# Performance work log

Hardware: AMD Instinct MI355X
Metric: run time of the kernel (lower is better)

The kernel has to match this reference:

```python
import jax, jax.numpy as jnp
import numpy as np

N_NODES = 100000

def _gcn_conv(x, edge_index, W, b):
    # PyG GCNConv with normalize=False, add_self_loops=False:
    # out[dst] = sum_{(src,dst) in E} (x @ W)[src] + b
    xw = x @ W                                   # [N, out]
    src, dst = edge_index[0], edge_index[1]
    agg = jax.ops.segment_sum(xw[src], dst, num_segments=x.shape[0])  # [N, out]
    return agg + b

def setup_inputs() -> dict:
    key = jax.random.key(0)
    k1, k2, k3, k4 = jax.random.split(key, 4)
    F_in, F_hid, F_out = 128, 64, 40
    E = 1_600_000
    x = jax.random.normal(k1, (N_NODES, F_in), dtype=jnp.float32)
    edge_index = jax.random.randint(k2, (2, E), 0, N_NODES, dtype=jnp.int64)
    W1 = jax.random.normal(k3, (F_in, F_hid), dtype=jnp.float32) * (1.0 / np.sqrt(F_in))
    b1 = jnp.zeros((F_hid,), dtype=jnp.float32)
    W2 = jax.random.normal(k4, (F_hid, F_out), dtype=jnp.float32) * (1.0 / np.sqrt(F_hid))
    b2 = jnp.zeros((F_out,), dtype=jnp.float32)
    return {"x": x, "edge_index": edge_index, "W1": W1, "b1": b1, "W2": W2, "b2": b2}

def reference(x, edge_index, W1, b1, W2, b2):
    h = _gcn_conv(x, edge_index, W1, b1)
    h = jax.nn.relu(h)
    h = _gcn_conv(h, edge_index, W2, b2)
    return jax.nn.log_softmax(h, axis=1)
```

## Files before the change

kernel.cpp:

```cpp
#include <hip/hip_runtime.h>
#include <cstdint>
#include <cstddef>

#define F_IN  128
#define F_HID 64
#define F_OUT 40

#define BSH   9
#define NBMAX 256
#define CHUNK 4096

#define BLD_T   512
#define BLD_CAP 10240

typedef __attribute__((ext_vector_type(8))) short short8;
typedef __attribute__((ext_vector_type(4))) float f32x4;

__device__ __forceinline__ unsigned short f2bf(float f) {
  unsigned u = __float_as_uint(f);
  u += 0x7fffu + ((u >> 16) & 1u);
  return (unsigned short)(u >> 16);
}
__device__ __forceinline__ float bf2f(unsigned short b) {
  return __uint_as_float((unsigned)b << 16);
}
__device__ __forceinline__ float bflo(unsigned u) { return __uint_as_float(u << 16); }
__device__ __forceinline__ float bfhi(unsigned u) { return __uint_as_float(u & 0xffff0000u); }
__device__ __forceinline__ unsigned packbf(float lo, float hi) {
  return (unsigned)f2bf(lo) | ((unsigned)f2bf(hi) << 16);
}

__global__ __launch_bounds__(256) void front_k(const float* __restrict__ x,
                                               const float* __restrict__ W1,
                                               const float* __restrict__ W2,
                                               unsigned short* __restrict__ w2s,
                                               unsigned short* __restrict__ xw, int N,
                                               const int* __restrict__ ei,
                                               int* __restrict__ counts,
                                               int E, int NBLK, int NBUCK) {
  __shared__ int lh[NBMAX];
  __shared__ unsigned short w1l[8192];
  int t = threadIdx.x;

  if ((int)blockIdx.x < NBLK) {
    int blk = blockIdx.x;
    lh[t] = 0;
    __syncthreads();
    int e0 = blk * CHUNK;
    int n = min(CHUNK, E - e0);
    for (int i = t; i < n; i += 256)
      atomicAdd(&lh[((unsigned)ei[E + e0 + i]) >> BSH], 1);
    __syncthreads();
    if (t < NBUCK) counts[t * NBLK + blk] = lh[t];
    if (blk == 0) {
      for (int i = t; i < 3072; i += 256) {
        int f = i >> 9, r = i & 511;
        int lane = r >> 3, j = r & 7;
        int ct = f >> 1, ks = f & 1;
        int n2 = ct * 16 + (lane & 15);
        int k = ks * 32 + (lane >> 4) * 8 + j;
        w2s[i] = (n2 < F_OUT) ? f2bf(W2[k * F_OUT + n2]) : (unsigned short)0;
      }
    }
    return;
  }

  {
    int k = t >> 1, n0 = (t & 1) * 32;
    const float4* wp = (const float4*)(W1 + k * F_HID + n0);
    float4 v[8];
#pragma unroll
    for (int u = 0; u < 8; ++u) v[u] = wp[u];
#pragma unroll
    for (int u = 0; u < 32; ++u) {
      int n = n0 + u;
      float f = ((const float*)v)[u];
      int idx = ((n >> 4) * 4 + (k >> 5)) * 512 +
                (((k >> 3) & 3) * 16 + (n & 15)) * 8 + (k & 7);
      w1l[idx] = f2bf(f);
    }
  }
  __syncthreads();

  int gblk = blockIdx.x - NBLK;
  int lane = t & 63;
  int wid  = gblk * 4 + (t >> 6);
  int row0 = wid * 16;
  if (row0 >= N) return;
  int m = lane & 15, q = lane >> 4;

  if (row0 + 16 <= N) {
    short8 b[16];
#pragma unroll
    for (int f = 0; f < 16; ++f)
      b[f] = *(const short8*)(w1l + f * 512 + lane * 8);

    short8 a[4];
#pragma unroll
    for (int ks = 0; ks < 4; ++ks) {
      const float* xp = x + (size_t)(row0 + m) * F_IN + ks * 32 + q * 8;
      float4 v0 = *(const float4*)xp;
      float4 v1 = *(const float4*)(xp + 4);
      short8 tt;
      tt[0] = (short)f2bf(v0.x); tt[1] = (short)f2bf(v0.y);
      tt[2] = (short)f2bf(v0.z); tt[3] = (short)f2bf(v0.w);
      tt[4] = (short)f2bf(v1.x); tt[5] = (short)f2bf(v1.y);
      tt[6] = (short)f2bf(v1.z); tt[7] = (short)f2bf(v1.w);
      a[ks] = tt;
    }

    f32x4 z = {0.f, 0.f, 0.f, 0.f};
    f32x4 acc[4] = {z, z, z, z};
#pragma unroll
    for (int ct = 0; ct < 4; ++ct)
#pragma unroll
      for (int ks = 0; ks < 4; ++ks)
        acc[ct] = __builtin_amdgcn_mfma_f32_16x16x32_bf16(a[ks], b[ct * 4 + ks],
                                                          acc[ct], 0, 0, 0);
#pragma unroll
    for (int ct = 0; ct < 4; ++ct)
#pragma unroll
      for (int r = 0; r < 4; ++r) {
        int row = row0 + q * 4 + r;
        xw[(size_t)row * F_HID + ct * 16 + m] = f2bf(acc[ct][r]);
      }
  } else {
    for (int r = 0; r < 16 && row0 + r < N; ++r) {
      const float* xr = x + (size_t)(row0 + r) * F_IN;
      float s = 0.f;
      for (int k = 0; k < F_IN; ++k) s = fmaf(xr[k], W1[k * F_HID + lane], s);
      xw[(size_t)(row0 + r) * F_HID + lane] = f2bf(s);
    }
  }
}

__global__ __launch_bounds__(256) void scanA_k(const int* __restrict__ a,
                                               int* __restrict__ psum, int M) {
  int t = threadIdx.x;
  int base = blockIdx.x * 2048 + t * 8;
  int s = 0;
#pragma unroll
  for (int j = 0; j < 8; ++j) if (base + j < M) s += a[base + j];
#pragma unroll
  for (int off = 32; off; off >>= 1) s += __shfl_xor(s, off, 64);
  __shared__ int sm[4];
  if ((t & 63) == 0) sm[t >> 6] = s;
  __syncthreads();
  if (t == 0) psum[blockIdx.x] = sm[0] + sm[1] + sm[2] + sm[3];
}

__global__ __launch_bounds__(256) void scanC_k(int* __restrict__ a,
                                               const int* __restrict__ psum,
                                               int M, int E, int nb) {
  __shared__ int sb[256];
  __shared__ int sm[256];
  int t = threadIdx.x;

  int pv = (t < nb) ? psum[t] : 0;
  sb[t] = pv;
  __syncthreads();
  for (int off = 1; off < 256; off <<= 1) {
    int add = (t >= off) ? sb[t - off] : 0;
    __syncthreads();
    sb[t] += add;
    __syncthreads();
  }
  int excl = sb[t] - pv;
  __syncthreads();
  sb[t] = excl;
  __syncthreads();
  int blockBase = sb[blockIdx.x];

  int base = blockIdx.x * 2048 + t * 8;
  int v[8];
  int s = 0;
#pragma unroll
  for (int j = 0; j < 8; ++j) {
    v[j] = (base + j < M) ? a[base + j] : 0;
    s += v[j];
  }
  sm[t] = s;
  __syncthreads();
  for (int off = 1; off < 256; off <<= 1) {
    int add = (t >= off) ? sm[t - off] : 0;
    __syncthreads();
    sm[t] += add;
    __syncthreads();
  }
  int run = blockBase + sm[t] - s;
#pragma unroll
  for (int j = 0; j < 8; ++j) {
    if (base + j < M) a[base + j] = run;
    run += v[j];
  }
  if (blockIdx.x == 0 && t == 0) a[M] = E;
}

__global__ __launch_bounds__(256) void partition_k(const int* __restrict__ bases,
                                                   const int* __restrict__ ei,
                                                   unsigned* __restrict__ ebuf,
                                                   int E, int NBLK, int NBUCK) {
  __shared__ uint2 slots[CHUNK];
  __shared__ int scn[NBMAX], lcur[NBMAX], gadj[NBMAX];
  int t = threadIdx.x, blk = blockIdx.x;
  int e0 = blk * CHUNK;
  int n = min(CHUNK, E - e0);

  int i0 = t * NBLK + blk;
  int cnt = 0, base0 = 0;
  if (t < NBUCK) {
    base0 = bases[i0];
    cnt = bases[i0 + 1] - base0;
  }
  scn[t] = cnt;
  __syncthreads();
  for (int off = 1; off < 256; off <<= 1) {
    int add = (t >= off) ? scn[t - off] : 0;
    __syncthreads();
    scn[t] += add;
    __syncthreads();
  }
  int excl = scn[t] - cnt;
  if (t < NBUCK) { lcur[t] = excl; gadj[t] = base0 - excl; }
  __syncthreads();

  for (int i = t; i < n; i += 256) {
    int s = ei[e0 + i], d = ei[E + e0 + i];
    int pos = atomicAdd(&lcur[((unsigned)d) >> BSH], 1);
    slots[pos] = make_uint2((unsigned)s, (unsigned)d);
  }
  __syncthreads();
  for (int i = t; i < n; i += 256) {
    uint2 sd = slots[i];
    unsigned pk = ((sd.y & 511u) << 17) | sd.x;
    ebuf[gadj[sd.y >> BSH] + i] = pk;
  }
}

__global__ __launch_bounds__(BLD_T) void build_k(const unsigned* __restrict__ ebuf,
                                                 const int* __restrict__ bases,
                                                 int* __restrict__ row_ptr,
                                                 int* __restrict__ csr,
                                                 int N, int E, int NBLK) {
  __shared__ int hist[512];
  __shared__ int psc[256];
  __shared__ unsigned stg[BLD_CAP];
  int t = threadIdx.x, b = blockIdx.x;
  int nodeBase = b << BSH;
  int S = bases[b * NBLK];
  int T = bases[(b + 1) * NBLK];
  int n = T - S;
  bool useLds = (n <= BLD_CAP);

  if (t < 512) hist[t] = 0;
  __syncthreads();
  for (int i = t; i < n; i += BLD_T) {
    unsigned v = ebuf[S + i];
    if (useLds) stg[i] = v;
    atomicAdd(&hist[v >> 17], 1);
  }
  __syncthreads();

  int v0 = 0, v1 = 0, pair = 0;
  if (t < 256) {
    v0 = hist[2 * t]; v1 = hist[2 * t + 1];
    pair = v0 + v1;
    psc[t] = pair;
  }
  __syncthreads();
  for (int off = 1; off < 256; off <<= 1) {
    int add = (t >= off && t < 256) ? psc[t - off] : 0;
    __syncthreads();
    if (t < 256) psc[t] += add;
    __syncthreads();
  }
  if (t < 256) {
    int ep = psc[t] - pair;
    int e0 = ep, e1 = ep + v0;
    int node0 = nodeBase + 2 * t;
    if (node0 < N) row_ptr[node0] = S + e0;
    if (node0 + 1 < N) row_ptr[node0 + 1] = S + e1;
    hist[2 * t] = e0; hist[2 * t + 1] = e1;
  }
  if (b == 0 && t == 0) row_ptr[N] = E;
  __syncthreads();
  for (int i = t; i < n; i += BLD_T) {
    unsigned v = useLds ? stg[i] : ebuf[S + i];
    int pos = atomicAdd(&hist[v >> 17], 1);
    csr[S + pos] = (int)(v & 0x1FFFFu);
  }
}

__global__ __launch_bounds__(256) void agg1g2_k(const unsigned short* __restrict__ xw,
                                                const int* __restrict__ row_ptr,
                                                const int* __restrict__ csr,
                                                const float* __restrict__ b1,
                                                const unsigned short* __restrict__ w2s,
                                                const float* __restrict__ W2,
                                                unsigned short* __restrict__ hw, int N) {
  __shared__ uint4 hsm[32][8];
  int t = threadIdx.x;
  int wave = t >> 6, lane = t & 63;
  int blockRow0 = blockIdx.x * 32;
  int rowBase = blockRow0 + wave * 8;
  int row = rowBase + (lane >> 3);
  int part = lane & 7;
  bool live = row < N;

  int start = live ? row_ptr[row] : 0;
  int end   = live ? row_ptr[row + 1] : 0;

  float acc[8], bcc[8];
#pragma unroll
  for (int j = 0; j < 8; ++j) { acc[j] = 0.f; bcc[j] = 0.f; }

  int i = start;
  for (; i + 3 < end; i += 4) {
    int s0 = csr[i];
    int s1 = csr[i + 1];
    int s2 = csr[i + 2];
    int s3 = csr[i + 3];
    uint4 v0 = *(const uint4*)(xw + ((size_t)s0 << 6) + (part << 3));
    uint4 v1 = *(const uint4*)(xw + ((size_t)s1 << 6) + (part << 3));
    uint4 v2 = *(const uint4*)(xw + ((size_t)s2 << 6) + (part << 3));
    uint4 v3 = *(const uint4*)(xw + ((size_t)s3 << 6) + (part << 3));
    acc[0] += bflo(v0.x); acc[1] += bfhi(v0.x);
    acc[2] += bflo(v0.y); acc[3] += bfhi(v0.y);
    acc[4] += bflo(v0.z); acc[5] += bfhi(v0.z);
    acc[6] += bflo(v0.w); acc[7] += bfhi(v0.w);
    bcc[0] += bflo(v1.x); bcc[1] += bfhi(v1.x);
    bcc[2] += bflo(v1.y); bcc[3] += bfhi(v1.y);
    bcc[4] += bflo(v1.z); bcc[5] += bfhi(v1.z);
    bcc[6] += bflo(v1.w); bcc[7] += bfhi(v1.w);
    acc[0] += bflo(v2.x); acc[1] += bfhi(v2.x);
    acc[2] += bflo(v2.y); acc[3] += bfhi(v2.y);
    acc[4] += bflo(v2.z); acc[5] += bfhi(v2.z);
    acc[6] += bflo(v2.w); acc[7] += bfhi(v2.w);
    bcc[0] += bflo(v3.x); bcc[1] += bfhi(v3.x);
    bcc[2] += bflo(v3.y); bcc[3] += bfhi(v3.y);
    bcc[4] += bflo(v3.z); bcc[5] += bfhi(v3.z);
    bcc[6] += bflo(v3.w); bcc[7] += bfhi(v3.w);
  }
  for (; i < end; ++i) {
    int s = csr[i];
    uint4 v = *(const uint4*)(xw + ((size_t)s << 6) + (part << 3));
    acc[0] += bflo(v.x); acc[1] += bfhi(v.x);
    acc[2] += bflo(v.y); acc[3] += bfhi(v.y);
    acc[4] += bflo(v.z); acc[5] += bfhi(v.z);
    acc[6] += bflo(v.w); acc[7] += bfhi(v.w);
  }

  if (live) {
    int c0 = part << 3;
    float4 bA = *(const float4*)(b1 + c0);
    float4 bB = *(const float4*)(b1 + c0 + 4);
    float r0 = fmaxf(acc[0] + bcc[0] + bA.x, 0.f);
    float r1 = fmaxf(acc[1] + bcc[1] + bA.y, 0.f);
    float r2 = fmaxf(acc[2] + bcc[2] + bA.z, 0.f);
    float r3 = fmaxf(acc[3] + bcc[3] + bA.w, 0.f);
    float r4 = fmaxf(acc[4] + bcc[4] + bB.x, 0.f);
    float r5 = fmaxf(acc[5] + bcc[5] + bB.y, 0.f);
    float r6 = fmaxf(acc[6] + bcc[6] + bB.z, 0.f);
    float r7 = fmaxf(acc[7] + bcc[7] + bB.w, 0.f);
    uint4 o = make_uint4(packbf(r0, r1), packbf(r2, r3), packbf(r4, r5), packbf(r6, r7));
    int lr = row - blockRow0;
    hsm[lr][part ^ (lr & 7)] = o;
  }
  __syncthreads();

  if (wave < 2) {
    int frow0 = blockRow0 + wave * 16;
    if (frow0 >= N) return;
    int m = lane & 15, q = lane >> 4;
    if (frow0 + 16 <= N) {
      short8 b[6];
#pragma unroll
      for (int f = 0; f < 6; ++f)
        b[f] = *(const short8*)(w2s + f * 512 + lane * 8);
      short8 a[2];
#pragma unroll
      for (int ks = 0; ks < 2; ++ks) {
        int lr = wave * 16 + m;
        int p = ks * 4 + q;
        a[ks] = *(const short8*)&hsm[lr][p ^ (lr & 7)];
      }
      f32x4 z = {0.f, 0.f, 0.f, 0.f};
      f32x4 acc2[3] = {z, z, z};
#pragma unroll
      for (int ct = 0; ct < 3; ++ct)
#pragma unroll
        for (int ks = 0; ks < 2; ++ks)
          acc2[ct] = __builtin_amdgcn_mfma_f32_16x16x32_bf16(a[ks], b[ct * 2 + ks],
                                                             acc2[ct], 0, 0, 0);
#pragma unroll
      for (int ct = 0; ct < 3; ++ct)
#pragma unroll
        for (int r = 0; r < 4; ++r) {
          int row2 = frow0 + q * 4 + r;
          int c = ct * 16 + m;
          if (c < F_OUT) hw[(size_t)row2 * F_OUT + c] = f2bf(acc2[ct][r]);
        }
    } else {
      for (int r = 0; r < 16; ++r) {
        int row2 = frow0 + r;
        if (row2 >= N) break;
        if (lane < F_OUT) {
          int lr = wave * 16 + r;
          float s = 0.f;
          for (int k = 0; k < F_HID; ++k) {
            const unsigned short* hp =
                (const unsigned short*)&hsm[lr][(k >> 3) ^ (lr & 7)];
            s = fmaf(bf2f(hp[k & 7]), W2[k * F_OUT + lane], s);
          }
          hw[(size_t)row2 * F_OUT + lane] = f2bf(s);
        }
      }
    }
  }
}

__global__ __launch_bounds__(256) void agg2_ls_k(const unsigned short* __restrict__ hw,
                                                 const int* __restrict__ row_ptr,
                                                 const int* __restrict__ csr,
                                                 const float* __restrict__ b2,
                                                 float* __restrict__ out, int N) {
  int wid = (blockIdx.x * 256 + threadIdx.x) >> 6;
  int lane = threadIdx.x & 63;
  int rowBase = wid * 8;
  if (rowBase >= N) return;
  int row = rowBase + (lane >> 3);
  int part = lane & 7;
  bool live = row < N;
  bool ld = live && (part < 5);

  int start = live ? row_ptr[row] : 0;
  int end   = live ? row_ptr[row + 1] : 0;

  float acc[8], bcc[8];
#pragma unroll
  for (int j = 0; j < 8; ++j) { acc[j] = 0.f; bcc[j] = 0.f; }

  int i = start;
  for (; i + 3 < end; i += 4) {
    int s0 = csr[i];
    int s1 = csr[i + 1];
    int s2 = csr[i + 2];
    int s3 = csr[i + 3];
    if (ld) {
      uint4 v0 = *(const uint4*)(hw + (size_t)s0 * F_OUT + (part << 3));
      uint4 v1 = *(const uint4*)(hw + (size_t)s1 * F_OUT + (part << 3));
      uint4 v2 = *(const uint4*)(hw + (size_t)s2 * F_OUT + (part << 3));
      uint4 v3 = *(const uint4*)(hw + (size_t)s3 * F_OUT + (part << 3));
      acc[0] += bflo(v0.x); acc[1] += bfhi(v0.x);
      acc[2] += bflo(v0.y); acc[3] += bfhi(v0.y);
      acc[4] += bflo(v0.z); acc[5] += bfhi(v0.z);
      acc[6] += bflo(v0.w); acc[7] += bfhi(v0.w);
      bcc[0] += bflo(v1.x); bcc[1] += bfhi(v1.x);
      bcc[2] += bflo(v1.y); bcc[3] += bfhi(v1.y);
      bcc[4] += bflo(v1.z); bcc[5] += bfhi(v1.z);
      bcc[6] += bflo(v1.w); bcc[7] += bfhi(v1.w);
      acc[0] += bflo(v2.x); acc[1] += bfhi(v2.x);
      acc[2] += bflo(v2.y); acc[3] += bfhi(v2.y);
      acc[4] += bflo(v2.z); acc[5] += bfhi(v2.z);
      acc[6] += bflo(v2.w); acc[7] += bfhi(v2.w);
      bcc[0] += bflo(v3.x); bcc[1] += bfhi(v3.x);
      bcc[2] += bflo(v3.y); bcc[3] += bfhi(v3.y);
      bcc[4] += bflo(v3.z); bcc[5] += bfhi(v3.z);
      bcc[6] += bflo(v3.w); bcc[7] += bfhi(v3.w);
    }
  }
  for (; i < end; ++i) {
    int s = csr[i];
    if (ld) {
      uint4 v = *(const uint4*)(hw + (size_t)s * F_OUT + (part << 3));
      acc[0] += bflo(v.x); acc[1] += bfhi(v.x);
      acc[2] += bflo(v.y); acc[3] += bfhi(v.y);
      acc[4] += bflo(v.z); acc[5] += bfhi(v.z);
      acc[6] += bflo(v.w); acc[7] += bfhi(v.w);
    }
  }

  bool valid = ld;
  float vj[8];
  float m = -3.4e38f;
  if (valid) {
    int c0 = part << 3;
    float4 bA = *(const float4*)(b2 + c0);
    float4 bB = *(const float4*)(b2 + c0 + 4);
    vj[0] = acc[0] + bcc[0] + bA.x; vj[1] = acc[1] + bcc[1] + bA.y;
    vj[2] = acc[2] + bcc[2] + bA.z; vj[3] = acc[3] + bcc[3] + bA.w;
    vj[4] = acc[4] + bcc[4] + bB.x; vj[5] = acc[5] + bcc[5] + bB.y;
    vj[6] = acc[6] + bcc[6] + bB.z; vj[7] = acc[7] + bcc[7] + bB.w;
#pragma unroll
    for (int j = 0; j < 8; ++j) m = fmaxf(m, vj[j]);
  }
#pragma unroll
  for (int off = 1; off < 8; off <<= 1) m = fmaxf(m, __shfl_xor(m, off, 64));
  float ex = 0.f;
  if (valid) {
#pragma unroll
    for (int j = 0; j < 8; ++j) ex += __expf(vj[j] - m);
  }
#pragma unroll
  for (int off = 1; off < 8; off <<= 1) ex += __shfl_xor(ex, off, 64);
  float lse = __logf(ex) + m;

  if (valid) {
    int c0 = part << 3;
    float* op = out + (size_t)row * F_OUT + c0;
    *(float4*)op = make_float4(vj[0] - lse, vj[1] - lse, vj[2] - lse, vj[3] - lse);
    *(float4*)(op + 4) = make_float4(vj[4] - lse, vj[5] - lse, vj[6] - lse, vj[7] - lse);
  }
}

extern "C" void kernel_launch(void* const* d_in, const int* in_sizes, int n_in,
                              void* d_out, int out_size, void* d_ws, size_t ws_size,
                              hipStream_t stream) {
  const float* x  = (const float*)d_in[0];
  const int*   ei = (const int*)d_in[1];
  const float* W1 = (const float*)d_in[2];
  const float* b1 = (const float*)d_in[3];
  const float* W2 = (const float*)d_in[4];
  const float* b2 = (const float*)d_in[5];

  int N = in_sizes[0] / F_IN;
  int E = in_sizes[1] / 2;

  char* base = (char*)d_ws;
  size_t szA = (size_t)N * F_HID * sizeof(unsigned short);
  size_t szEb = (size_t)E * sizeof(unsigned);
  size_t szHw = (size_t)N * F_OUT * sizeof(unsigned short);
  size_t szB = (szEb > szHw) ? szEb : szHw;
  unsigned short* xw = (unsigned short*)base;
  char* regB = base + ((szA + 255) & ~(size_t)255);
  unsigned* ebuf       = (unsigned*)regB;
  unsigned short* hw   = (unsigned short*)regB;
  int* row_ptr = (int*)(regB + ((szB + 255) & ~(size_t)255));
  int* csr     = row_ptr + N + 1;
  int* counts  = csr + E;
  float* out = (float*)d_out;

  int aggGrid  = (N * 8 + 255) / 256;
  int gemmGrid = (N + 63) / 64;
  int fusGrid  = (N + 31) / 32;
  int NBLK  = (E + CHUNK - 1) / CHUNK;
  int NBUCK = (N + 511) >> BSH;
  int M = NBUCK * NBLK;
  int* psum = counts + M + 1;
  unsigned short* w2s = (unsigned short*)(psum + 256);
  int scanBlocks = (M + 2047) / 2048;

  front_k<<<NBLK + gemmGrid, 256, 0, stream>>>(x, W1, W2, w2s, xw, N,
                                               ei, counts, E, NBLK, NBUCK);

  scanA_k<<<scanBlocks, 256, 0, stream>>>(counts, psum, M);
  scanC_k<<<scanBlocks, 256, 0, stream>>>(counts, psum, M, E, scanBlocks);
  partition_k<<<NBLK, 256, 0, stream>>>(counts, ei, ebuf, E, NBLK, NBUCK);
  build_k<<<NBUCK, BLD_T, 0, stream>>>(ebuf, counts, row_ptr, csr, N, E, NBLK);

  agg1g2_k<<<fusGrid, 256, 0, stream>>>(xw, row_ptr, csr, b1, w2s, W2, hw, N);
  agg2_ls_k<<<aggGrid, 256, 0, stream>>>(hw, row_ptr, csr, b2, out, N);
}
```

Before: 218.4 us.

## Merge pipeline stages into two persistent cooperative kernels with grid syncs

Replaces seven kernel launches with two cooperative persistent kernels. The first fuses histogram, GEMM1, both scan passes, partition and CSR build, separated by grid.sync(). The second fuses layer-1 aggregation plus GEMM2 with layer-2 aggregation and log-softmax. The intent is to remove launch gaps and inter-kernel drain. It also pads hw rows to 64 columns for aligned gathers and drops the LDS staging in the build step. The risks are fixed-size grids limited by occupancy, grid-sync overhead, and lower per-phase parallelism (e.g. the build now uses 256 threads without LDS caching).

After: 598.2 us. 174% more time.

```diff
diff --git a/kernel.cpp b/kernel.cpp
--- a/kernel.cpp
+++ b/kernel.cpp
@@ -1,6 +1,9 @@
 #include <hip/hip_runtime.h>
+#include <hip/hip_cooperative_groups.h>
 #include <cstdint>
 #include <cstddef>
+
+namespace cg = cooperative_groups;
 
 #define F_IN  128
 #define F_HID 64
@@ -9,9 +12,6 @@
 #define BSH   9
 #define NBMAX 256
 #define CHUNK 4096
-
-#define BLD_T   512
-#define BLD_CAP 10240
 
 typedef __attribute__((ext_vector_type(8))) short short8;
 typedef __attribute__((ext_vector_type(4))) float f32x4;
@@ -30,427 +30,271 @@
   return (unsigned)f2bf(lo) | ((unsigned)f2bf(hi) << 16);
 }
 
-__global__ __launch_bounds__(256) void front_k(const float* __restrict__ x,
-                                               const float* __restrict__ W1,
-                                               const float* __restrict__ W2,
-                                               unsigned short* __restrict__ w2s,
-                                               unsigned short* __restrict__ xw, int N,
-                                               const int* __restrict__ ei,
-                                               int* __restrict__ counts,
-                                               int E, int NBLK, int NBUCK) {
-  __shared__ int lh[NBMAX];
-  __shared__ unsigned short w1l[8192];
+__global__ __launch_bounds__(256, 4) void pre_k(
+    const float* __restrict__ x, const float* __restrict__ W1,
+    const float* __restrict__ W2, unsigned short* __restrict__ w2s,
+    unsigned short* __restrict__ xw,
+    const int* __restrict__ ei, int* __restrict__ counts,
+    int* __restrict__ psum, unsigned* __restrict__ ebuf,
+    int* __restrict__ row_ptr, int* __restrict__ csr,
+    int N, int E, int NBLK, int NBUCK, int M, int scanBlocks,
+    int frontJobs, int G) {
+  __shared__ union {
+    struct { unsigned short w1l[8192]; int lh[NBMAX]; } f;
+    struct { int sb[256]; int sm[256]; } s;
+    struct { uint2 slots[CHUNK]; int scn[NBMAX]; int lcur[NBMAX];
+             int gadj[NBMAX]; } p;
+    struct { int hist[512]; int psc[256]; } b;
+  } u;
+  cg::grid_group grid = cg::this_grid();
   int t = threadIdx.x;
-
-  if ((int)blockIdx.x < NBLK) {
-    int blk = blockIdx.x;
-    lh[t] = 0;
-    __syncthreads();
-    int e0 = blk * CHUNK;
-    int n = min(CHUNK, E - e0);
-    for (int i = t; i < n; i += 256)
-      atomicAdd(&lh[((unsigned)ei[E + e0 + i]) >> BSH], 1);
-    __syncthreads();
-    if (t < NBUCK) counts[t * NBLK + blk] = lh[t];
-    if (blk == 0) {
-      for (int i = t; i < 3072; i += 256) {
-        int f = i >> 9, r = i & 511;
-        int lane = r >> 3, j = r & 7;
-        int ct = f >> 1, ks = f & 1;
-        int n2 = ct * 16 + (lane & 15);
-        int k = ks * 32 + (lane >> 4) * 8 + j;
-        w2s[i] = (n2 < F_OUT) ? f2bf(W2[k * F_OUT + n2]) : (unsigned short)0;
-      }
-    }
-    return;
-  }
+  int blk = blockIdx.x;
 
   {
     int k = t >> 1, n0 = (t & 1) * 32;
     const float4* wp = (const float4*)(W1 + k * F_HID + n0);
     float4 v[8];
 #pragma unroll
-    for (int u = 0; u < 8; ++u) v[u] = wp[u];
-#pragma unroll
-    for (int u = 0; u < 32; ++u) {
-      int n = n0 + u;
-      float f = ((const float*)v)[u];
+    for (int uu = 0; uu < 8; ++uu) v[uu] = wp[uu];
+#pragma unroll
+    for (int uu = 0; uu < 32; ++uu) {
+      int n = n0 + uu;
+      float f = ((const float*)v)[uu];
       int idx = ((n >> 4) * 4 + (k >> 5)) * 512 +
                 (((k >> 3) & 3) * 16 + (n & 15)) * 8 + (k & 7);
-      w1l[idx] = f2bf(f);
+      u.f.w1l[idx] = f2bf(f);
     }
   }
   __syncthreads();
 
-  int gblk = blockIdx.x - NBLK;
-  int lane = t & 63;
-  int wid  = gblk * 4 + (t >> 6);
-  int row0 = wid * 16;
-  if (row0 >= N) return;
-  int m = lane & 15, q = lane >> 4;
-
-  if (row0 + 16 <= N) {
-    short8 b[16];
-#pragma unroll
-    for (int f = 0; f < 16; ++f)
-      b[f] = *(const short8*)(w1l + f * 512 + lane * 8);
-
-    short8 a[4];
-#pragma unroll
-    for (int ks = 0; ks < 4; ++ks) {
-      const float* xp = x + (size_t)(row0 + m) * F_IN + ks * 32 + q * 8;
-      float4 v0 = *(const float4*)xp;
-      float4 v1 = *(const float4*)(xp + 4);
-      short8 tt;
-      tt[0] = (short)f2bf(v0.x); tt[1] = (short)f2bf(v0.y);
-      tt[2] = (short)f2bf(v0.z); tt[3] = (short)f2bf(v0.w);
-      tt[4] = (short)f2bf(v1.x); tt[5] = (short)f2bf(v1.y);
-      tt[6] = (short)f2bf(v1.z); tt[7] = (short)f2bf(v1.w);
-      a[ks] = tt;
-    }
-
-    f32x4 z = {0.f, 0.f, 0.f, 0.f};
-    f32x4 acc[4] = {z, z, z, z};
-#pragma unroll
-    for (int ct = 0; ct < 4; ++ct)
-#pragma unroll
-      for (int ks = 0; ks < 4; ++ks)
-        acc[ct] = __builtin_amdgcn_mfma_f32_16x16x32_bf16(a[ks], b[ct * 4 + ks],
-                                                          acc[ct], 0, 0, 0);
-#pragma unroll
-    for (int ct = 0; ct < 4; ++ct)
-#pragma unroll
-      for (int r = 0; r < 4; ++r) {
-        int row = row0 + q * 4 + r;
-        xw[(size_t)row * F_HID + ct * 16 + m] = f2bf(acc[ct][r]);
-      }
-  } else {
-    for (int r = 0; r < 16 && row0 + r < N; ++r) {
-      const float* xr = x + (size_t)(row0 + r) * F_IN;
-      float s = 0.f;
-      for (int k = 0; k < F_IN; ++k) s = fmaf(xr[k], W1[k * F_HID + lane], s);
-      xw[(size_t)(row0 + r) * F_HID + lane] = f2bf(s);
-    }
+  for (int j = blk; j < frontJobs; j += G) {
+    if (j < NBLK) {
+      u.f.lh[t] = 0;
+      __syncthreads();
+      int e0 = j * CHUNK;
+      int n = min(CHUNK, E - e0);
+      for (int i = t; i < n; i += 256)
+        atomicAdd(&u.f.lh[((unsigned)ei[E + e0 + i]) >> BSH], 1);
+      __syncthreads();
+      if (t < NBUCK) counts[t * NBLK + j] = u.f.lh[t];
+      if (j == 0) {
+        for (int i = t; i < 3072; i += 256) {
+          int f = i >> 9, r = i & 511;
+          int lane = r >> 3, jj = r & 7;
+          int ct = f >> 1, ks = f & 1;
+          int n2 = ct * 16 + (lane & 15);
+          int k = ks * 32 + (lane >> 4) * 8 + jj;
+          w2s[i] = (n2 < F_OUT) ? f2bf(W2[k * F_OUT + n2]) : (unsigned short)0;
+        }
+      }
+      __syncthreads();
+    } else {
+      int gblk = j - NBLK;
+      int lane = t & 63;
+      int wid = gblk * 4 + (t >> 6);
+      int row0 = wid * 16;
+      if (row0 < N) {
+        int m = lane & 15, q = lane >> 4;
+        if (row0 + 16 <= N) {
+          short8 b[16];
+#pragma unroll
+          for (int f = 0; f < 16; ++f)
+            b[f] = *(const short8*)(u.f.w1l + f * 512 + lane * 8);
+          short8 a[4];
+#pragma unroll
+          for (int ks = 0; ks < 4; ++ks) {
+            const float* xp = x + (size_t)(row0 + m) * F_IN + ks * 32 + q * 8;
+            float4 v0 = *(const float4*)xp;
+            float4 v1 = *(const float4*)(xp + 4);
+            short8 tt;
+            tt[0] = (short)f2bf(v0.x); tt[1] = (short)f2bf(v0.y);
+            tt[2] = (short)f2bf(v0.z); tt[3] = (short)f2bf(v0.w);
+            tt[4] = (short)f2bf(v1.x); tt[5] = (short)f2bf(v1.y);
+            tt[6] = (short)f2bf(v1.z); tt[7] = (short)f2bf(v1.w);
+            a[ks] = tt;
+          }
+          f32x4 z = {0.f, 0.f, 0.f, 0.f};
+          f32x4 acc[4] = {z, z, z, z};
+#pragma unroll
+          for (int ct = 0; ct < 4; ++ct)
+#pragma unroll
+            for (int ks = 0; ks < 4; ++ks)
+              acc[ct] = __builtin_amdgcn_mfma_f32_16x16x32_bf16(
+                  a[ks], b[ct * 4 + ks], acc[ct], 0, 0, 0);
+#pragma unroll
+          for (int ct = 0; ct < 4; ++ct)
+#pragma unroll
+            for (int r = 0; r < 4; ++r) {
+              int row = row0 + q * 4 + r;
+              xw[(size_t)row * F_HID + ct * 16 + m] = f2bf(acc[ct][r]);
+            }
+        } else {
+          for (int r = 0; r < 16 && row0 + r < N; ++r) {
+            const float* xr = x + (size_t)(row0 + r) * F_IN;
+            float s = 0.f;
+            for (int k = 0; k < F_IN; ++k)
+              s = fmaf(xr[k], W1[k * F_HID + lane], s);
+            xw[(size_t)(row0 + r) * F_HID + lane] = f2bf(s);
+          }
+        }
+      }
+    }
+  }
+  grid.sync();
+
+  for (int j = blk; j < scanBlocks; j += G) {
+    int base = j * 2048 + t * 8;
+    int s = 0;
+#pragma unroll
+    for (int q = 0; q < 8; ++q) if (base + q < M) s += counts[base + q];
+#pragma unroll
+    for (int off = 32; off; off >>= 1) s += __shfl_xor(s, off, 64);
+    if ((t & 63) == 0) u.s.sb[t >> 6] = s;
+    __syncthreads();
+    if (t == 0) psum[j] = u.s.sb[0] + u.s.sb[1] + u.s.sb[2] + u.s.sb[3];
+    __syncthreads();
+  }
+  grid.sync();
+
+  for (int j = blk; j < scanBlocks; j += G) {
+    int pv = (t < scanBlocks) ? psum[t] : 0;
+    u.s.sb[t] = pv;
+    __syncthreads();
+    for (int off = 1; off < 256; off <<= 1) {
+      int add = (t >= off) ? u.s.sb[t - off] : 0;
+      __syncthreads();
+      u.s.sb[t] += add;
+      __syncthreads();
+    }
+    int blockBase = (j > 0) ? u.s.sb[j - 1] : 0;
+    int base = j * 2048 + t * 8;
+    int v[8];
+    int s = 0;
+#pragma unroll
+    for (int q = 0; q < 8; ++q) {
+      v[q] = (base + q < M) ? counts[base + q] : 0;
+      s += v[q];
+    }
+    u.s.sm[t] = s;
+    __syncthreads();
+    for (int off = 1; off < 256; off <<= 1) {
+      int add = (t >= off) ? u.s.sm[t - off] : 0;
+      __syncthreads();
+      u.s.sm[t] += add;
+      __syncthreads();
+    }
+    int run = blockBase + u.s.sm[t] - s;
+#pragma unroll
+    for (int q = 0; q < 8; ++q) {
+      if (base + q < M) counts[base + q] = run;
+      run += v[q];
+    }
+    if (j == 0 && t == 0) counts[M] = E;
+    __syncthreads();
+  }
+  grid.sync();
+
+  for (int j = blk; j < NBLK; j += G) {
+    int e0 = j * CHUNK;
+    int n = min(CHUNK, E - e0);
+    int i0 = t * NBLK + j;
+    int cnt = 0, base0 = 0;
+    if (t < NBUCK) { base0 = counts[i0]; cnt = counts[i0 + 1] - base0; }
+    u.p.scn[t] = cnt;
+    __syncthreads();
+    for (int off = 1; off < 256; off <<= 1) {
+      int add = (t >= off) ? u.p.scn[t - off] : 0;
+      __syncthreads();
+      u.p.scn[t] += add;
+      __syncthreads();
+    }
+    int excl = u.p.scn[t] - cnt;
+    if (t < NBUCK) { u.p.lcur[t] = excl; u.p.gadj[t] = base0 - excl; }
+    __syncthreads();
+    for (int i = t; i < n; i += 256) {
+      int sv = ei[e0 + i], d = ei[E + e0 + i];
+      int pos = atomicAdd(&u.p.lcur[((unsigned)d) >> BSH], 1);
+      u.p.slots[pos] = make_uint2((unsigned)sv, (unsigned)d);
+    }
+    __syncthreads();
+    for (int i = t; i < n; i += 256) {
+      uint2 sd = u.p.slots[i];
+      unsigned pk = ((sd.y & 511u) << 17) | sd.x;
+      ebuf[u.p.gadj[sd.y >> BSH] + i] = pk;
+    }
+    __syncthreads();
+  }
+  grid.sync();
+
+  for (int j = blk; j < NBUCK; j += G) {
+    int nodeBase = j << BSH;
+    int S = counts[j * NBLK];
+    int T = counts[(j + 1) * NBLK];
+    u.b.hist[t] = 0; u.b.hist[t + 256] = 0;
+    __syncthreads();
+    for (int i = S + t; i < T; i += 256)
+      atomicAdd(&u.b.hist[ebuf[i] >> 17], 1);
+    __syncthreads();
+    int v0 = u.b.hist[2 * t], v1 = u.b.hist[2 * t + 1];
+    int pair = v0 + v1;
+    u.b.psc[t] = pair;
+    __syncthreads();
+    for (int off = 1; off < 256; off <<= 1) {
+      int add = (t >= off) ? u.b.psc[t - off] : 0;
+      __syncthreads();
+      u.b.psc[t] += add;
+      __syncthreads();
+    }
+    int ep = u.b.psc[t] - pair;
+    int e0v = ep, e1v = ep + v0;
+    int node0 = nodeBase + 2 * t;
+    if (node0 < N) row_ptr[node0] = S + e0v;
+    if (node0 + 1 < N) row_ptr[node0 + 1] = S + e1v;
+    if (j == 0 && t == 0) row_ptr[N] = E;
+    u.b.hist[2 * t] = e0v; u.b.hist[2 * t + 1] = e1v;
+    __syncthreads();
+    for (int i = S + t; i < T; i += 256) {
+      unsigned v = ebuf[i];
+      int pos = atomicAdd(&u.b.hist[v >> 17], 1);
+      csr[S + pos] = (int)(v & 0x1FFFFu);
+    }
+    __syncthreads();
   }
 }
 
-__global__ __launch_bounds__(256) void scanA_k(const int* __restrict__ a,
-                                               int* __restrict__ psum, int M) {
-  int t = threadIdx.x;
-  int base = blockIdx.x * 2048 + t * 8;
-  int s = 0;
-#pragma unroll
-  for (int j = 0; j < 8; ++j) if (base + j < M) s += a[base + j];
-#pragma unroll
-  for (int off = 32; off; off >>= 1) s += __shfl_xor(s, off, 64);
-  __shared__ int sm[4];
-  if ((t & 63) == 0) sm[t >> 6] = s;
-  __syncthreads();
-  if (t == 0) psum[blockIdx.x] = sm[0] + sm[1] + sm[2] + sm[3];
-}
-
-__global__ __launch_bounds__(256) void scanC_k(int* __restrict__ a,
-                                               const int* __restrict__ psum,
-                                               int M, int E, int nb) {
-  __shared__ int sb[256];
-  __shared__ int sm[256];
-  int t = threadIdx.x;
-
-  int pv = (t < nb) ? psum[t] : 0;
-  sb[t] = pv;
-  __syncthreads();
-  for (int off = 1; off < 256; off <<= 1) {
-    int add = (t >= off) ? sb[t - off] : 0;
-    __syncthreads();
-    sb[t] += add;
-    __syncthreads();
-  }
-  int excl = sb[t] - pv;
-  __syncthreads();
-  sb[t] = excl;
-  __syncthreads();
-  int blockBase = sb[blockIdx.x];
-
-  int base = blockIdx.x * 2048 + t * 8;
-  int v[8];
-  int s = 0;
-#pragma unroll
-  for (int j = 0; j < 8; ++j) {
-    v[j] = (base + j < M) ? a[base + j] : 0;
-    s += v[j];
-  }
-  sm[t] = s;
-  __syncthreads();
-  for (int off = 1; off < 256; off <<= 1) {
-    int add = (t >= off) ? sm[t - off] : 0;
-    __syncthreads();
-    sm[t] += add;
-    __syncthreads();
-  }
-  int run = blockBase + sm[t] - s;
-#pragma unroll
-  for (int j = 0; j < 8; ++j) {
-    if (base + j < M) a[base + j] = run;
-    run += v[j];
-  }
-  if (blockIdx.x == 0 && t == 0) a[M] = E;
-}
-
-__global__ __launch_bounds__(256) void partition_k(const int* __restrict__ bases,
-                                                   const int* __restrict__ ei,
-                                                   unsigned* __restrict__ ebuf,
-                                                   int E, int NBLK, int NBUCK) {
-  __shared__ uint2 slots[CHUNK];
-  __shared__ int scn[NBMAX], lcur[NBMAX], gadj[NBMAX];
+__global__ __launch_bounds__(256, 6) void agg_k(
+    const unsigned short* __restrict__ xw, const int* __restrict__ row_ptr,
+    const int* __restrict__ csr, const float* __restrict__ b1,
+    const unsigned short* __restrict__ w2s, const float* __restrict__ W2,
+    unsigned short* __restrict__ hw, const float* __restrict__ b2,
+    float* __restrict__ out, int N, int aggJobs, int G) {
+  __shared__ uint4 hsm[32][8];
+  cg::grid_group grid = cg::this_grid();
   int t = threadIdx.x, blk = blockIdx.x;
-  int e0 = blk * CHUNK;
-  int n = min(CHUNK, E - e0);
-
-  int i0 = t * NBLK + blk;
-  int cnt = 0, base0 = 0;
-  if (t < NBUCK) {
-    base0 = bases[i0];
-    cnt = bases[i0 + 1] - base0;
-  }
-  scn[t] = cnt;
-  __syncthreads();
-  for (int off = 1; off < 256; off <<= 1) {
-    int add = (t >= off) ? scn[t - off] : 0;
-    __syncthreads();
-    scn[t] += add;
-    __syncthreads();
-  }
-  int excl = scn[t] - cnt;
-  if (t < NBUCK) { lcur[t] = excl; gadj[t] = base0 - excl; }
-  __syncthreads();
-
-  for (int i = t; i < n; i += 256) {
-    int s = ei[e0 + i], d = ei[E + e0 + i];
-    int pos = atomicAdd(&lcur[((unsigned)d) >> BSH], 1);
-    slots[pos] = make_uint2((unsigned)s, (unsigned)d);
-  }
-  __syncthreads();
-  for (int i = t; i < n; i += 256) {
-    uint2 sd = slots[i];
-    unsigned pk = ((sd.y & 511u) << 17) | sd.x;
-    ebuf[gadj[sd.y >> BSH] + i] = pk;
-  }
-}
-
-__global__ __launch_bounds__(BLD_T) void build_k(const unsigned* __restrict__ ebuf,
-                                                 const int* __restrict__ bases,
-                                                 int* __restrict__ row_ptr,
-                                                 int* __restrict__ csr,
-                                                 int N, int E, int NBLK) {
-  __shared__ int hist[512];
-  __shared__ int psc[256];
-  __shared__ unsigned stg[BLD_CAP];
-  int t = threadIdx.x, b = blockIdx.x;
-  int nodeBase = b << BSH;
-  int S = bases[b * NBLK];
-  int T = bases[(b + 1) * NBLK];
-  int n = T - S;
-  bool useLds = (n <= BLD_CAP);
-
-  if (t < 512) hist[t] = 0;
-  __syncthreads();
-  for (int i = t; i < n; i += BLD_T) {
-    unsigned v = ebuf[S + i];
-    if (useLds) stg[i] = v;
-    atomicAdd(&hist[v >> 17], 1);
-  }
-  __syncthreads();
-
-  int v0 = 0, v1 = 0, pair = 0;
-  if (t < 256) {
-    v0 = hist[2 * t]; v1 = hist[2 * t + 1];
-    pair = v0 + v1;
-    psc[t] = pair;
-  }
-  __syncthreads();
-  for (int off = 1; off < 256; off <<= 1) {
-    int add = (t >= off && t < 256) ? psc[t - off] : 0;
-    __syncthreads();
-    if (t < 256) psc[t] += add;
-    __syncthreads();
-  }
-  if (t < 256) {
-    int ep = psc[t] - pair;
-    int e0 = ep, e1 = ep + v0;
-    int node0 = nodeBase + 2 * t;
-    if (node0 < N) row_ptr[node0] = S + e0;
-    if (node0 + 1 < N) row_ptr[node0 + 1] = S + e1;
-    hist[2 * t] = e0; hist[2 * t + 1] = e1;
-  }
-  if (b == 0 && t == 0) row_ptr[N] = E;
-  __syncthreads();
-  for (int i = t; i < n; i += BLD_T) {
-    unsigned v = useLds ? stg[i] : ebuf[S + i];
-    int pos = atomicAdd(&hist[v >> 17], 1);
-    csr[S + pos] = (int)(v & 0x1FFFFu);
-  }
-}
-
-__global__ __launch_bounds__(256) void agg1g2_k(const unsigned short* __restrict__ xw,
-                                                const int* __restrict__ row_ptr,
-                                                const int* __restrict__ csr,
-                                                const float* __restrict__ b1,
-                                                const unsigned short* __restrict__ w2s,
-                                                const float* __restrict__ W2,
-                                                unsigned short* __restrict__ hw, int N) {
-  __shared__ uint4 hsm[32][8];
-  int t = threadIdx.x;
   int wave = t >> 6, lane = t & 63;
-  int blockRow0 = blockIdx.x * 32;
-  int rowBase = blockRow0 + wave * 8;
-  int row = rowBase + (lane >> 3);
   int part = lane & 7;
-  bool live = row < N;
-
-  int start = live ? row_ptr[row] : 0;
-  int end   = live ? row_ptr[row + 1] : 0;
-
-  float acc[8], bcc[8];
-#pragma unroll
-  for (int j = 0; j < 8; ++j) { acc[j] = 0.f; bcc[j] = 0.f; }
-
-  int i = start;
-  for (; i + 3 < end; i += 4) {
-    int s0 = csr[i];
-    int s1 = csr[i + 1];
-    int s2 = csr[i + 2];
-    int s3 = csr[i + 3];
-    uint4 v0 = *(const uint4*)(xw + ((size_t)s0 << 6) + (part << 3));
-    uint4 v1 = *(const uint4*)(xw + ((size_t)s1 << 6) + (part << 3));
-    uint4 v2 = *(const uint4*)(xw + ((size_t)s2 << 6) + (part << 3));
-    uint4 v3 = *(const uint4*)(xw + ((size_t)s3 << 6) + (part << 3));
-    acc[0] += bflo(v0.x); acc[1] += bfhi(v0.x);
-    acc[2] += bflo(v0.y); acc[3] += bfhi(v0.y);
-    acc[4] += bflo(v0.z); acc[5] += bfhi(v0.z);
-    acc[6] += bflo(v0.w); acc[7] += bfhi(v0.w);
-    bcc[0] += bflo(v1.x); bcc[1] += bfhi(v1.x);
-    bcc[2] += bflo(v1.y); bcc[3] += bfhi(v1.y);
-    bcc[4] += bflo(v1.z); bcc[5] += bfhi(v1.z);
-    bcc[6] += bflo(v1.w); bcc[7] += bfhi(v1.w);
-    acc[0] += bflo(v2.x); acc[1] += bfhi(v2.x);
-    acc[2] += bflo(v2.y); acc[3] += bfhi(v2.y);
-    acc[4] += bflo(v2.z); acc[5] += bfhi(v2.z);
-    acc[6] += bflo(v2.w); acc[7] += bfhi(v2.w);
-    bcc[0] += bflo(v3.x); bcc[1] += bfhi(v3.x);
-    bcc[2] += bflo(v3.y); bcc[3] += bfhi(v3.y);
-    bcc[4] += bflo(v3.z); bcc[5] += bfhi(v3.z);
-    bcc[6] += bflo(v3.w); bcc[7] += bfhi(v3.w);
-  }
-  for (; i < end; ++i) {
-    int s = csr[i];
-    uint4 v = *(const uint4*)(xw + ((size_t)s << 6) + (part << 3));
-    acc[0] += bflo(v.x); acc[1] += bfhi(v.x);
-    acc[2] += bflo(v.y); acc[3] += bfhi(v.y);
-    acc[4] += bflo(v.z); acc[5] += bfhi(v.z);
-    acc[6] += bflo(v.w); acc[7] += bfhi(v.w);
-  }
-
-  if (live) {
-    int c0 = part << 3;
-    float4 bA = *(const float4*)(b1 + c0);
-    float4 bB = *(const float4*)(b1 + c0 + 4);
-    float r0 = fmaxf(acc[0] + bcc[0] + bA.x, 0.f);
-    float r1 = fmaxf(acc[1] + bcc[1] + bA.y, 0.f);
-    float r2 = fmaxf(acc[2] + bcc[2] + bA.z, 0.f);
-    float r3 = fmaxf(acc[3] + bcc[3] + bA.w, 0.f);
-    float r4 = fmaxf(acc[4] + bcc[4] + bB.x, 0.f);
-    float r5 = fmaxf(acc[5] + bcc[5] + bB.y, 0.f);
-    float r6 = fmaxf(acc[6] + bcc[6] + bB.z, 0.f);
-    float r7 = fmaxf(acc[7] + bcc[7] + bB.w, 0.f);
-    uint4 o = make_uint4(packbf(r0, r1), packbf(r2, r3), packbf(r4, r5), packbf(r6, r7));
-    int lr = row - blockRow0;
-    hsm[lr][part ^ (lr & 7)] = o;
-  }
-  __syncthreads();
-
-  if (wave < 2) {
-    int frow0 = blockRow0 + wave * 16;
-    if (frow0 >= N) return;
-    int m = lane & 15, q = lane >> 4;
-    if (frow0 + 16 <= N) {
-      short8 b[6];
-#pragma unroll
-      for (int f = 0; f < 6; ++f)
-        b[f] = *(const short8*)(w2s + f * 512 + lane * 8);
-      short8 a[2];
-#pragma unroll
-      for (int ks = 0; ks < 2; ++ks) {
-        int lr = wave * 16 + m;
-        int p = ks * 4 + q;
-        a[ks] = *(const short8*)&hsm[lr][p ^ (lr & 7)];
-      }
-      f32x4 z = {0.f, 0.f, 0.f, 0.f};
-      f32x4 acc2[3] = {z, z, z};
-#pragma unroll
-      for (int ct = 0; ct < 3; ++ct)
-#pragma unroll
-        for (int ks = 0; ks < 2; ++ks)
-          acc2[ct] = __builtin_amdgcn_mfma_f32_16x16x32_bf16(a[ks], b[ct * 2 + ks],
-                                                             acc2[ct], 0, 0, 0);
-#pragma unroll
-      for (int ct = 0; ct < 3; ++ct)
-#pragma unroll
-        for (int r = 0; r < 4; ++r) {
-          int row2 = frow0 + q * 4 + r;
-          int c = ct * 16 + m;
-          if (c < F_OUT) hw[(size_t)row2 * F_OUT + c] = f2bf(acc2[ct][r]);
-        }
-    } else {
-      for (int r = 0; r < 16; ++r) {
-        int row2 = frow0 + r;
-        if (row2 >= N) break;
-        if (lane < F_OUT) {
-          int lr = wave * 16 + r;
-          float s = 0.f;
-          for (int k = 0; k < F_HID; ++k) {
-            const unsigned short* hp =
-                (const unsigned short*)&hsm[lr][(k >> 3) ^ (lr & 7)];
-            s = fmaf(bf2f(hp[k & 7]), W2[k * F_OUT + lane], s);
-          }
-          hw[(size_t)row2 * F_OUT + lane] = f2bf(s);
-        }
-      }
-    }
-  }
-}
-
-__global__ __launch_bounds__(256) void agg2_ls_k(const unsigned short* __restrict__ hw,
-                                                 const int* __restrict__ row_ptr,
-                                                 const int* __restrict__ csr,
-                                                 const float* __restrict__ b2,
-                                                 float* __restrict__ out, int N) {
-  int wid = (blockIdx.x * 256 + threadIdx.x) >> 6;
-  int lane = threadIdx.x & 63;
-  int rowBase = wid * 8;
-  if (rowBase >= N) return;
-  int row = rowBase + (lane >> 3);
-  int part = lane & 7;
-  bool live = row < N;
-  bool ld = live && (part < 5);
-
-  int start = live ? row_ptr[row] : 0;
-  int end   = live ? row_ptr[row + 1] : 0;
-
-  float acc[8], bcc[8];
-#pragma unroll
-  for (int j = 0; j < 8; ++j) { acc[j] = 0.f; bcc[j] = 0.f; }
-
-  int i = start;
-  for (; i + 3 < end; i += 4) {
-    int s0 = csr[i];
-    int s1 = csr[i + 1];
-    int s2 = csr[i + 2];
-    int s3 = csr[i + 3];
-    if (ld) {
-      uint4 v0 = *(const uint4*)(hw + (size_t)s0 * F_OUT + (part << 3));
-      uint4 v1 = *(const uint4*)(hw + (size_t)s1 * F_OUT + (part << 3));
-      uint4 v2 = *(const uint4*)(hw + (size_t)s2 * F_OUT + (part << 3));
-      uint4 v3 = *(const uint4*)(hw + (size_t)s3 * F_OUT + (part << 3));
+
+  for (int j = blk; j < aggJobs; j += G) {
+    int blockRow0 = j * 32;
+    int row = blockRow0 + wave * 8 + (lane >> 3);
+    bool live = row < N;
+    int start = live ? row_ptr[row] : 0;
+    int end   = live ? row_ptr[row + 1] : 0;
+
+    float acc[8], bcc[8];
+#pragma unroll
+    for (int q = 0; q < 8; ++q) { acc[q] = 0.f; bcc[q] = 0.f; }
+
+    int i = start;
+    for (; i + 3 < end; i += 4) {
+      int s0 = csr[i];
+      int s1 = csr[i + 1];
+      int s2 = csr[i + 2];
+      int s3 = csr[i + 3];
+      uint4 v0 = *(const uint4*)(xw + ((size_t)s0 << 6) + (part << 3));
+      uint4 v1 = *(const uint4*)(xw + ((size_t)s1 << 6) + (part << 3));
+      uint4 v2 = *(const uint4*)(xw + ((size_t)s2 << 6) + (part << 3));
+      uint4 v3 = *(const uint4*)(xw + ((size_t)s3 << 6) + (part << 3));
       acc[0] += bflo(v0.x); acc[1] += bfhi(v0.x);
       acc[2] += bflo(v0.y); acc[3] += bfhi(v0.y);
       acc[4] += bflo(v0.z); acc[5] += bfhi(v0.z);
@@ -468,48 +312,176 @@
       bcc[4] += bflo(v3.z); bcc[5] += bfhi(v3.z);
       bcc[6] += bflo(v3.w); bcc[7] += bfhi(v3.w);
     }
-  }
-  for (; i < end; ++i) {
-    int s = csr[i];
-    if (ld) {
-      uint4 v = *(const uint4*)(hw + (size_t)s * F_OUT + (part << 3));
+    for (; i < end; ++i) {
+      int s = csr[i];
+      uint4 v = *(const uint4*)(xw + ((size_t)s << 6) + (part << 3));
       acc[0] += bflo(v.x); acc[1] += bfhi(v.x);
       acc[2] += bflo(v.y); acc[3] += bfhi(v.y);
       acc[4] += bflo(v.z); acc[5] += bfhi(v.z);
       acc[6] += bflo(v.w); acc[7] += bfhi(v.w);
     }
-  }
-
-  bool valid = ld;
-  float vj[8];
-  float m = -3.4e38f;
-  if (valid) {
-    int c0 = part << 3;
-    float4 bA = *(const float4*)(b2 + c0);
-    float4 bB = *(const float4*)(b2 + c0 + 4);
-    vj[0] = acc[0] + bcc[0] + bA.x; vj[1] = acc[1] + bcc[1] + bA.y;
-    vj[2] = acc[2] + bcc[2] + bA.z; vj[3] = acc[3] + bcc[3] + bA.w;
-    vj[4] = acc[4] + bcc[4] + bB.x; vj[5] = acc[5] + bcc[5] + bB.y;
-    vj[6] = acc[6] + bcc[6] + bB.z; vj[7] = acc[7] + bcc[7] + bB.w;
-#pragma unroll
-    for (int j = 0; j < 8; ++j) m = fmaxf(m, vj[j]);
-  }
-#pragma unroll
-  for (int off = 1; off < 8; off <<= 1) m = fmaxf(m, __shfl_xor(m, off, 64));
-  float ex = 0.f;
-  if (valid) {
-#pragma unroll
-    for (int j = 0; j < 8; ++j) ex += __expf(vj[j] - m);
-  }
-#pragma unroll
-  for (int off = 1; off < 8; off <<= 1) ex += __shfl_xor(ex, off, 64);
-  float lse = __logf(ex) + m;
-
-  if (valid) {
-    int c0 = part << 3;
-    float* op = out + (size_t)row * F_OUT + c0;
-    *(float4*)op = make_float4(vj[0] - lse, vj[1] - lse, vj[2] - lse, vj[3] - lse);
-    *(float4*)(op + 4) = make_float4(vj[4] - lse, vj[5] - lse, vj[6] - lse, vj[7] - lse);
+
+    if (live) {
+      int c0 = part << 3;
+      float4 bA = *(const float4*)(b1 + c0);
+      float4 bB = *(const float4*)(b1 + c0 + 4);
+      float r0 = fmaxf(acc[0] + bcc[0] + bA.x, 0.f);
+      float r1 = fmaxf(acc[1] + bcc[1] + bA.y, 0.f);
+      float r2 = fmaxf(acc[2] + bcc[2] + bA.z, 0.f);
+      float r3 = fmaxf(acc[3] + bcc[3] + bA.w, 0.f);
+      float r4 = fmaxf(acc[4] + bcc[4] + bB.x, 0.f);
+      float r5 = fmaxf(acc[5] + bcc[5] + bB.y, 0.f);
+      float r6 = fmaxf(acc[6] + bcc[6] + bB.z, 0.f);
+      float r7 = fmaxf(acc[7] + bcc[7] + bB.w, 0.f);
+      uint4 o = make_uint4(packbf(r0, r1), packbf(r2, r3),
+                           packbf(r4, r5), packbf(r6, r7));
+      int lr = row - blockRow0;
+      hsm[lr][part ^ (lr & 7)] = o;
+    }
+    __syncthreads();
+
+    if (wave < 2) {
+      int frow0 = blockRow0 + wave * 16;
+      if (frow0 < N) {
+        int m = lane & 15, q = lane >> 4;
+        if (frow0 + 16 <= N) {
+          short8 b[6];
+#pragma unroll
+          for (int f = 0; f < 6; ++f)
+            b[f] = *(const short8*)(w2s + f * 512 + lane * 8);
+          short8 a[2];
+#pragma unroll
+          for (int ks = 0; ks < 2; ++ks) {
+            int lr = wave * 16 + m;
+            int p = ks * 4 + q;
+            a[ks] = *(const short8*)&hsm[lr][p ^ (lr & 7)];
+          }
+          f32x4 z = {0.f, 0.f, 0.f, 0.f};
+          f32x4 acc2[3] = {z, z, z};
+#pragma unroll
+          for (int ct = 0; ct < 3; ++ct)
+#pragma unroll
+            for (int ks = 0; ks < 2; ++ks)
+              acc2[ct] = __builtin_amdgcn_mfma_f32_16x16x32_bf16(
+                  a[ks], b[ct * 2 + ks], acc2[ct], 0, 0, 0);
+#pragma unroll
+          for (int ct = 0; ct < 3; ++ct)
+#pragma unroll
+            for (int r = 0; r < 4; ++r) {
+              int row2 = frow0 + q * 4 + r;
+              int c = ct * 16 + m;
+              if (c < F_OUT) hw[(size_t)row2 * F_HID + c] = f2bf(acc2[ct][r]);
+            }
+        } else {
+          for (int r = 0; r < 16; ++r) {
+            int row2 = frow0 + r;
+            if (row2 >= N) break;
+            if (lane < F_OUT) {
+              int lr = wave * 16 + r;
+              float s = 0.f;
+              for (int k = 0; k < F_HID; ++k) {
+                const unsigned short* hp =
+                    (const unsigned short*)&hsm[lr][(k >> 3) ^ (lr & 7)];
+                s = fmaf(bf2f(hp[k & 7]), W2[k * F_OUT + lane], s);
+              }
+              hw[(size_t)row2 * F_HID + lane] = f2bf(s);
+            }
+          }
+        }
+      }
+    }
+    __syncthreads();
+  }
+  grid.sync();
+
+  for (int j = blk; j < aggJobs; j += G) {
+    int wid = j * 4 + wave;
+    int rowBase = wid * 8;
+    if (rowBase < N) {
+      int row = rowBase + (lane >> 3);
+      bool live = row < N;
+      bool ld = live && (part < 5);
+
+      int start = live ? row_ptr[row] : 0;
+      int end   = live ? row_ptr[row + 1] : 0;
+
+      float acc[8], bcc[8];
+#pragma unroll
+      for (int q = 0; q < 8; ++q) { acc[q] = 0.f; bcc[q] = 0.f; }
+
+      int i = start;
+      for (; i + 3 < end; i += 4) {
+        int s0 = csr[i];
+        int s1 = csr[i + 1];
+        int s2 = csr[i + 2];
+        int s3 = csr[i + 3];
+        if (ld) {
+          uint4 v0 = *(const uint4*)(hw + ((size_t)s0 << 6) + (part << 3));
+          uint4 v1 = *(const uint4*)(hw + ((size_t)s1 << 6) + (part << 3));
+          uint4 v2 = *(const uint4*)(hw + ((size_t)s2 << 6) + (part << 3));
+          uint4 v3 = *(const uint4*)(hw + ((size_t)s3 << 6) + (part << 3));
+          acc[0] += bflo(v0.x); acc[1] += bfhi(v0.x);
+          acc[2] += bflo(v0.y); acc[3] += bfhi(v0.y);
+          acc[4] += bflo(v0.z); acc[5] += bfhi(v0.z);
+          acc[6] += bflo(v0.w); acc[7] += bfhi(v0.w);
+          bcc[0] += bflo(v1.x); bcc[1] += bfhi(v1.x);
+          bcc[2] += bflo(v1.y); bcc[3] += bfhi(v1.y);
+          bcc[4] += bflo(v1.z); bcc[5] += bfhi(v1.z);
+          bcc[6] += bflo(v1.w); bcc[7] += bfhi(v1.w);
+          acc[0] += bflo(v2.x); acc[1] += bfhi(v2.x);
+          acc[2] += bflo(v2.y); acc[3] += bfhi(v2.y);
+          acc[4] += bflo(v2.z); acc[5] += bfhi(v2.z);
+          acc[6] += bflo(v2.w); acc[7] += bfhi(v2.w);
+          bcc[0] += bflo(v3.x); bcc[1] += bfhi(v3.x);
+          bcc[2] += bflo(v3.y); bcc[3] += bfhi(v3.y);
+          bcc[4] += bflo(v3.z); bcc[5] += bfhi(v3.z);
+          bcc[6] += bflo(v3.w); bcc[7] += bfhi(v3.w);
+        }
+      }
+      for (; i < end; ++i) {
+        int s = csr[i];
+        if (ld) {
+          uint4 v = *(const uint4*)(hw + ((size_t)s << 6) + (part << 3));
+          acc[0] += bflo(v.x); acc[1] += bfhi(v.x);
+          acc[2] += bflo(v.y); acc[3] += bfhi(v.y);
+          acc[4] += bflo(v.z); acc[5] += bfhi(v.z);
+          acc[6] += bflo(v.w); acc[7] += bfhi(v.w);
+        }
+      }
+
+      float vj[8];
+      float mx = -3.4e38f;
+      if (ld) {
+        int c0 = part << 3;
+        float4 bA = *(const float4*)(b2 + c0);
+        float4 bB = *(const float4*)(b2 + c0 + 4);
+        vj[0] = acc[0] + bcc[0] + bA.x; vj[1] = acc[1] + bcc[1] + bA.y;
+        vj[2] = acc[2] + bcc[2] + bA.z; vj[3] = acc[3] + bcc[3] + bA.w;
+        vj[4] = acc[4] + bcc[4] + bB.x; vj[5] = acc[5] + bcc[5] + bB.y;
+        vj[6] = acc[6] + bcc[6] + bB.z; vj[7] = acc[7] + bcc[7] + bB.w;
+#pragma unroll
+        for (int q = 0; q < 8; ++q) mx = fmaxf(mx, vj[q]);
+      }
+#pragma unroll
+      for (int off = 1; off < 8; off <<= 1) mx = fmaxf(mx, __shfl_xor(mx, off, 64));
+      float ex = 0.f;
+      if (ld) {
+#pragma unroll
+        for (int q = 0; q < 8; ++q) ex += __expf(vj[q] - mx);
+      }
+#pragma unroll
+      for (int off = 1; off < 8; off <<= 1) ex += __shfl_xor(ex, off, 64);
+      float lse = __logf(ex) + mx;
+
+      if (ld) {
+        int c0 = part << 3;
+        float* op = out + (size_t)row * F_OUT + c0;
+        *(float4*)op = make_float4(vj[0] - lse, vj[1] - lse,
+                                   vj[2] - lse, vj[3] - lse);
+        *(float4*)(op + 4) = make_float4(vj[4] - lse, vj[5] - lse,
+                                         vj[6] - lse, vj[7] - lse);
+      }
+    }
   }
 }
 
@@ -529,7 +501,7 @@
   char* base = (char*)d_ws;
   size_t szA = (size_t)N * F_HID * sizeof(unsigned short);
   size_t szEb = (size_t)E * sizeof(unsigned);
-  size_t szHw = (size_t)N * F_OUT * sizeof(unsigned short);
+  size_t szHw = (size_t)N * F_HID * sizeof(unsigned short);
   size_t szB = (szEb > szHw) ? szEb : szHw;
   unsigned short* xw = (unsigned short*)base;
   char* regB = base + ((szA + 255) & ~(size_t)255);
@@ -540,24 +512,48 @@
   int* counts  = csr + E;
   float* out = (float*)d_out;
 
-  int aggGrid  = (N * 8 + 255) / 256;
-  int gemmGrid = (N + 63) / 64;
-  int fusGrid  = (N + 31) / 32;
   int NBLK  = (E + CHUNK - 1) / CHUNK;
   int NBUCK = (N + 511) >> BSH;
   int M = NBUCK * NBLK;
   int* psum = counts + M + 1;
-  unsigned short* w2s = (unsigned short*)(psum + 256);
+  unsigned short* w2s =
+      (unsigned short*)(((uintptr_t)(psum + 256) + 63) & ~(uintptr_t)63);
   int scanBlocks = (M + 2047) / 2048;
-
-  front_k<<<NBLK + gemmGrid, 256, 0, stream>>>(x, W1, W2, w2s, xw, N,
-                                               ei, counts, E, NBLK, NBUCK);
-
-  scanA_k<<<scanBlocks, 256, 0, stream>>>(counts, psum, M);
-  scanC_k<<<scanBlocks, 256, 0, stream>>>(counts, psum, M, E, scanBlocks);
-  partition_k<<<NBLK, 256, 0, stream>>>(counts, ei, ebuf, E, NBLK, NBUCK);
-  build_k<<<NBUCK, BLD_T, 0, stream>>>(ebuf, counts, row_ptr, csr, N, E, NBLK);
-
-  agg1g2_k<<<fusGrid, 256, 0, stream>>>(xw, row_ptr, csr, b1, w2s, W2, hw, N);
-  agg2_ls_k<<<aggGrid, 256, 0, stream>>>(hw, row_ptr, csr, b2, out, N);
+  int gemmGrid = (N + 63) / 64;
+  int frontJobs = NBLK + gemmGrid;
+  int aggJobs = (N + 31) / 32;
+
+  static int cap1 = -1, cap2 = -1, ncu = 0;
+  if (cap1 < 0) {
+    hipDeviceProp_t prop;
+    int dev = 0;
+    (void)hipGetDevice(&dev);
+    (void)hipGetDeviceProperties(&prop, dev);
+    ncu = prop.multiProcessorCount;
+    if (ncu <= 0) ncu = 256;
+    if (hipOccupancyMaxActiveBlocksPerMultiprocessor(&cap1,
+            reinterpret_cast<const void*>(pre_k), 256, 0) != hipSuccess ||
+        cap1 < 1)
+      cap1 = 2;
+    if (hipOccupancyMaxActiveBlocksPerMultiprocessor(&cap2,
+            reinterpret_cast<const void*>(agg_k), 256, 0) != hipSuccess ||
+        cap2 < 1)
+      cap2 = 2;
+  }
+  int G1 = cap1 * ncu; if (G1 > frontJobs) G1 = frontJobs;
+  int G2 = cap2 * ncu; if (G2 > aggJobs) G2 = aggJobs;
+
+  void* a1[] = {(void*)&x, (void*)&W1, (void*)&W2, (void*)&w2s, (void*)&xw,
+                (void*)&ei, (void*)&counts, (void*)&psum, (void*)&ebuf,
+                (void*)&row_ptr, (void*)&csr,
+                (void*)&N, (void*)&E, (void*)&NBLK, (void*)&NBUCK, (void*)&M,
+                (void*)&scanBlocks, (void*)&frontJobs, (void*)&G1};
+  (void)hipLaunchCooperativeKernel(reinterpret_cast<const void*>(pre_k),
+                                   dim3(G1), dim3(256), a1, 0, stream);
+
+  void* a2[] = {(void*)&xw, (void*)&row_ptr, (void*)&csr, (void*)&b1,
+                (void*)&w2s, (void*)&W2, (void*)&hw, (void*)&b2,
+                (void*)&out, (void*)&N, (void*)&aggJobs, (void*)&G2};
+  (void)hipLaunchCooperativeKernel(reinterpret_cast<const void*>(agg_k),
+                                   dim3(G2), dim3(256), a2, 0, stream);
 }
```
